# Performance work log

Measured on AMD Instinct MI355X. Metric: run time of the kernel, lower is better.

Reference implementation:

```python
import jax, jax.numpy as jnp
import numpy as np

B, S, D = 1, 2048, 1024
NH, NKV, HD = 16, 4, 64
N_REP = NH // NKV


def _rope_tables(seq_len, half_dim, base=10000.0):
    inv_freq = 1.0 / (base ** (np.arange(0, half_dim, dtype=np.float32) / half_dim))
    t = np.arange(seq_len, dtype=np.float32)
    freqs = np.outer(t, inv_freq)  # (S, HD//2)
    return jnp.asarray(np.cos(freqs)), jnp.asarray(np.sin(freqs))


def setup_inputs() -> dict:
    key = jax.random.key(0)
    ks = jax.random.split(key, 5)
    x = jax.random.normal(ks[0], (B, S, D), dtype=jnp.float32)
    rope_cos, rope_sin = _rope_tables(S, HD // 2)
    sd = 1.0 / np.sqrt(D)
    Wq = jax.random.normal(ks[1], (D, NH * HD), dtype=jnp.float32) * sd
    Wk = jax.random.normal(ks[2], (D, NKV * HD), dtype=jnp.float32) * sd
    Wv = jax.random.normal(ks[3], (D, NKV * HD), dtype=jnp.float32) * sd
    Wo = jax.random.normal(ks[4], (NH * HD, D), dtype=jnp.float32) * sd
    return {"x": x, "rope_cos": rope_cos, "rope_sin": rope_sin,
            "Wq": Wq, "Wk": Wk, "Wv": Wv, "Wo": Wo}


def _apply_rope(t, cos, sin):
    # t: (B, H, S, HD); cos/sin: (S, HD//2). Rotate-half convention.
    t1, t2 = jnp.split(t, 2, axis=-1)
    c = cos[None, None, :, :]
    s = sin[None, None, :, :]
    return jnp.concatenate([t1 * c - t2 * s, t2 * c + t1 * s], axis=-1)


def reference(x, rope_cos, rope_sin, Wq, Wk, Wv, Wo):
    b, s, _ = x.shape
    # projections -> (B, H, S, HD)
    q = (x @ Wq).reshape(b, s, NH, HD).transpose(0, 2, 1, 3)
    k = (x @ Wk).reshape(b, s, NKV, HD).transpose(0, 2, 1, 3)
    v = (x @ Wv).reshape(b, s, NKV, HD).transpose(0, 2, 1, 3)
    q = _apply_rope(q, rope_cos, rope_sin)
    k = _apply_rope(k, rope_cos, rope_sin)
    # GQA expansion (repeat_interleave on head axis)
    k = jnp.repeat(k, N_REP, axis=1)
    v = jnp.repeat(v, N_REP, axis=1)
    scale = HD ** -0.5
    scores = jnp.einsum('bhqd,bhkd->bhqk', q, k) * scale
    causal = jnp.tril(jnp.ones((s, s), dtype=bool))
    scores = jnp.where(causal[None, None], scores, jnp.float32(-jnp.inf))
    attn = jax.nn.softmax(scores, axis=-1)
    out = jnp.einsum('bhqk,bhkd->bhqd', attn, v)  # (B, H, S, HD)
    out = out.transpose(0, 2, 1, 3).reshape(b, s, NH * HD)
    return out @ Wo
```

## Files before the change

### kernel.cpp

```cpp
#include <hip/hip_runtime.h>

typedef unsigned short ushort_t;
typedef __attribute__((ext_vector_type(8))) short short8;
typedef __attribute__((ext_vector_type(4))) float f32x4;
typedef __attribute__((ext_vector_type(4))) unsigned short ushort4v;
typedef __attribute__((ext_vector_type(8))) unsigned short ushort8v;

#define S_LEN 2048
#define D_MODEL 1024
#define NH 16
#define NKV 4
#define HD 64

__device__ __forceinline__ ushort_t f2bf(float f) {
    unsigned u = __float_as_uint(f);
    u += 0x7fffu + ((u >> 16) & 1u);
    return (ushort_t)(u >> 16);
}

__device__ __forceinline__ void cp16(void* lds, const void* g) {
    __builtin_amdgcn_global_load_lds(
        (__attribute__((address_space(1))) void*)g,
        (__attribute__((address_space(3))) void*)lds, 16, 0, 0);
}

__global__ __launch_bounds__(256) void prep_kernel(
    const float* __restrict__ x, ushort_t* __restrict__ xb,
    const float* __restrict__ Wq, const float* __restrict__ Wk,
    const float* __restrict__ Wv, const float* __restrict__ Wo,
    ushort_t* __restrict__ WqT, ushort_t* __restrict__ WkT,
    ushort_t* __restrict__ WvT, ushort_t* __restrict__ WoT)
{
    const int t = threadIdx.x;
    if (blockIdx.z == 4) {
        const int b  = blockIdx.y * 16 + blockIdx.x;
        const int i0 = (b * 256 + t) * 4;
        #pragma unroll
        for (int rep = 0; rep < 8; ++rep) {
            const int i = i0 + rep * 262144;
            float4 v = *(const float4*)(x + i);
            ushort4v o = { f2bf(v.x), f2bf(v.y), f2bf(v.z), f2bf(v.w) };
            *(ushort4v*)(xb + i) = o;
        }
        return;
    }
    __shared__ ushort_t T[64 * 72];
    const float* W; ushort_t* WT; int N;
    switch (blockIdx.z) {
        case 0:  W = Wq; WT = WqT; N = 1024; break;
        case 1:  W = Wk; WT = WkT; N = 256;  break;
        case 2:  W = Wv; WT = WvT; N = 256;  break;
        default: W = Wo; WT = WoT; N = 1024; break;
    }
    const int n0 = blockIdx.y * 64;
    if (n0 >= N) return;
    const int k0 = blockIdx.x * 64;
    const int kr = t >> 4, nc = (t & 15) * 4;
    #pragma unroll
    for (int p = 0; p < 4; ++p) {
        const int k = kr + p * 16;
        float4 v = *(const float4*)(W + (size_t)(k0 + k) * N + n0 + nc);
        T[(nc + 0) * 72 + k] = f2bf(v.x);
        T[(nc + 1) * 72 + k] = f2bf(v.y);
        T[(nc + 2) * 72 + k] = f2bf(v.z);
        T[(nc + 3) * 72 + k] = f2bf(v.w);
    }
    __syncthreads();
    const int n = t >> 2, seg = (t & 3) * 16;
    ushort8v a = *(ushort8v*)&T[n * 72 + seg];
    ushort8v b = *(ushort8v*)&T[n * 72 + seg + 8];
    *(ushort8v*)(WT + (size_t)(n0 + n) * 1024 + k0 + seg)     = a;
    *(ushort8v*)(WT + (size_t)(n0 + n) * 1024 + k0 + seg + 8) = b;
}

__global__ __launch_bounds__(256, 2) void gemm_qkv_mfma(
    const ushort_t* __restrict__ xb, const ushort_t* __restrict__ WqT,
    const ushort_t* __restrict__ WkT, const ushort_t* __restrict__ WvT,
    const float* __restrict__ rc, const float* __restrict__ rs,
    ushort_t* __restrict__ Qb, ushort_t* __restrict__ Kb,
    ushort_t* __restrict__ Vtb)
{
    __shared__ ushort_t As[2][64 * 64];
    __shared__ ushort_t Bs[2][128 * 64];

    const int t = threadIdx.x;
    const int lane = t & 63, wave = t >> 6;
    const int wr = wave >> 1, wc = wave & 1;
    const int quad = lane >> 4, l15 = lane & 15;
    const int lq = lane >> 3, lr = lane & 7;
    const int swz_st = (lr ^ lq) * 8;
    const int l7 = l15 & 7;
    const int fsw0 = (quad ^ l7) * 8;
    const int fsw1 = ((quad + 4) ^ l7) * 8;

    const int m0 = blockIdx.x * 64;
    const int cy = blockIdx.y;

    const ushort_t* WT; int nloc;
    if (cy < 8)       { WT = WqT; nloc = cy * 128; }
    else if (cy < 10) { WT = WkT; nloc = (cy - 8) * 128; }
    else              { WT = WvT; nloc = (cy - 10) * 128; }

    f32x4 acc[2][4];
    #pragma unroll
    for (int i = 0; i < 2; ++i)
        #pragma unroll
        for (int j = 0; j < 4; ++j) acc[i][j] = (f32x4)0.f;

    auto stage = [&](int buf, int k0) {
        #pragma unroll
        for (int i = 0; i < 2; ++i) {
            const int r = wave * 16 + i * 8 + lq;
            cp16(&As[buf][(wave * 16 + i * 8) * 64],
                 xb + (size_t)(m0 + r) * 1024 + k0 + swz_st);
        }
        #pragma unroll
        for (int i = 0; i < 4; ++i) {
            const int r = wave * 32 + i * 8 + lq;
            cp16(&Bs[buf][(wave * 32 + i * 8) * 64],
                 WT + (size_t)(nloc + r) * 1024 + k0 + swz_st);
        }
    };

    stage(0, 0);
    __syncthreads();

    for (int kk = 0; kk < 16; ++kk) {
        const int cur = kk & 1;
        if (kk + 1 < 16) stage(cur ^ 1, (kk + 1) * 64);

        const ushort_t* Ac = &As[cur][0];
        const ushort_t* Bc = &Bs[cur][0];
        #pragma unroll
        for (int h = 0; h < 2; ++h) {
            const int fsw = h ? fsw1 : fsw0;
            short8 av[2], bv[4];
            #pragma unroll
            for (int i = 0; i < 2; ++i)
                av[i] = *(const short8*)&Ac[(wr * 32 + i * 16 + l15) * 64 + fsw];
            #pragma unroll
            for (int j = 0; j < 4; ++j)
                bv[j] = *(const short8*)&Bc[(wc * 64 + j * 16 + l15) * 64 + fsw];
            #pragma unroll
            for (int i = 0; i < 2; ++i)
                #pragma unroll
                for (int j = 0; j < 4; ++j)
                    acc[i][j] = __builtin_amdgcn_mfma_f32_16x16x32_bf16(
                        av[i], bv[j], acc[i][j], 0, 0, 0);
        }
        __syncthreads();
    }

    if (cy < 10) {
        ushort_t* dst = (cy < 8) ? Qb : Kb;
        const int h = ((cy < 8) ? cy : (cy - 8)) * 2 + wc;
        #pragma unroll
        for (int i = 0; i < 2; ++i) {
            #pragma unroll
            for (int j = 0; j < 2; ++j) {
                const int d = j * 16 + l15;
                #pragma unroll
                for (int reg = 0; reg < 4; ++reg) {
                    const int s = m0 + wr * 32 + i * 16 + quad * 4 + reg;
                    const float c  = rc[s * 32 + d];
                    const float sn = rs[s * 32 + d];
                    const float v1 = acc[i][j][reg];
                    const float v2 = acc[i][j + 2][reg];
                    dst[((size_t)h * S_LEN + s) * HD + d]      = f2bf(v1 * c - v2 * sn);
                    dst[((size_t)h * S_LEN + s) * HD + d + 32] = f2bf(v2 * c + v1 * sn);
                }
            }
        }
    } else {
        const int vh = (cy - 10) * 2 + wc;
        #pragma unroll
        for (int i = 0; i < 2; ++i) {
            const int s0 = m0 + wr * 32 + i * 16 + quad * 4;
            #pragma unroll
            for (int j = 0; j < 4; ++j) {
                const int d = j * 16 + l15;
                ushort4v o = { f2bf(acc[i][j][0]), f2bf(acc[i][j][1]),
                               f2bf(acc[i][j][2]), f2bf(acc[i][j][3]) };
                *(ushort4v*)&Vtb[((size_t)vh * HD + d) * S_LEN + s0] = o;
            }
        }
    }
}

__global__ __launch_bounds__(256, 2) void attn_mfma(
    const ushort_t* __restrict__ Qb, const ushort_t* __restrict__ Kb,
    const ushort_t* __restrict__ Vtb, ushort_t* __restrict__ attnb)
{
    __shared__ ushort_t Ks[2][2][64 * 64];
    __shared__ ushort_t Vs[2][2][64 * 64];
    __shared__ ushort_t Ps[4][16 * 72];

    const int t = threadIdx.x;
    const int lane = t & 63, wave = t >> 6;
    const int quad = lane >> 4, l15 = lane & 15;
    const int lq = lane >> 3, lr = lane & 7;
    const int swz_st = (lr ^ lq) * 8;
    const int l7 = l15 & 7;
    const int fsw0 = (quad ^ l7) * 8;
    const int fsw1 = ((quad + 4) ^ l7) * 8;

    const int h  = blockIdx.x;
    const int y  = blockIdx.y;
    const int qt = (y < 16) ? y : 47 - y;
    const int q0 = qt * 64;
    const int kvh = h >> 2;
    const int qrow0 = q0 + wave * 16;

    const ushort_t* Qg = Qb + ((size_t)h * S_LEN + qrow0) * HD;
    const ushort_t* Kg = Kb + (size_t)kvh * S_LEN * HD;
    const ushort_t* Vg = Vtb + (size_t)kvh * HD * S_LEN;

    short8 aq0 = *(const short8*)(Qg + (size_t)l15 * HD + quad * 8);
    short8 aq1 = *(const short8*)(Qg + (size_t)l15 * HD + 32 + quad * 8);

    float ps4[4] = {0.f, 0.f, 0.f, 0.f};
    f32x4 Oacc[4];
    #pragma unroll
    for (int jb = 0; jb < 4; ++jb) Oacc[jb] = (f32x4)0.f;

    const int nround = (qt + 2) >> 1;

    auto stage = [&](int buf, int kvbase) {
        #pragma unroll
        for (int u = 0; u < 2; ++u)
            #pragma unroll
            for (int i = 0; i < 2; ++i) {
                const int r = wave * 16 + i * 8 + lq;
                cp16(&Ks[buf][u][(wave * 16 + i * 8) * 64],
                     Kg + (size_t)(kvbase + u * 64 + r) * 64 + swz_st);
                cp16(&Vs[buf][u][(wave * 16 + i * 8) * 64],
                     Vg + (size_t)r * 2048 + kvbase + u * 64 + swz_st);
            }
    };

    stage(0, 0);
    __syncthreads();

    ushort_t* Pw = &Ps[wave][0];

    for (int round = 0; round < nround; ++round) {
        const int cur = round & 1;
        if (round + 1 < nround) stage(cur ^ 1, (round + 1) * 128);

        #pragma unroll
        for (int u = 0; u < 2; ++u) {
            const int kv0 = round * 128 + u * 64;
            if (kv0 > q0 + 63) break;
            const ushort_t* Kc = &Ks[cur][u][0];
            const ushort_t* Vc = &Vs[cur][u][0];

            f32x4 sv[4];
            #pragma unroll
            for (int jb = 0; jb < 4; ++jb) {
                short8 b0 = *(const short8*)&Kc[(jb * 16 + l15) * 64 + fsw0];
                short8 b1 = *(const short8*)&Kc[(jb * 16 + l15) * 64 + fsw1];
                f32x4 z = (f32x4)0.f;
                z = __builtin_amdgcn_mfma_f32_16x16x32_bf16(aq0, b0, z, 0, 0, 0);
                z = __builtin_amdgcn_mfma_f32_16x16x32_bf16(aq1, b1, z, 0, 0, 0);
                sv[jb] = z;
            }

            const bool diag = (kv0 == q0);
            #pragma unroll
            for (int jb = 0; jb < 4; ++jb) {
                const int col = kv0 + jb * 16 + l15;
                #pragma unroll
                for (int reg = 0; reg < 4; ++reg) {
                    float e = __expf(sv[jb][reg] * 0.125f);
                    if (diag && col > qrow0 + quad * 4 + reg) e = 0.f;
                    sv[jb][reg] = e;
                    ps4[reg] += e;
                }
            }

            #pragma unroll
            for (int jb = 0; jb < 4; ++jb)
                #pragma unroll
                for (int reg = 0; reg < 4; ++reg)
                    Pw[(quad * 4 + reg) * 72 + jb * 16 + l15] = f2bf(sv[jb][reg]);
            short8 p0 = *(const short8*)&Pw[l15 * 72 + quad * 8];
            short8 p1 = *(const short8*)&Pw[l15 * 72 + 32 + quad * 8];

            #pragma unroll
            for (int jb = 0; jb < 4; ++jb) {
                short8 v0 = *(const short8*)&Vc[(jb * 16 + l15) * 64 + fsw0];
                short8 v1 = *(const short8*)&Vc[(jb * 16 + l15) * 64 + fsw1];
                Oacc[jb] = __builtin_amdgcn_mfma_f32_16x16x32_bf16(p0, v0, Oacc[jb], 0, 0, 0);
                Oacc[jb] = __builtin_amdgcn_mfma_f32_16x16x32_bf16(p1, v1, Oacc[jb], 0, 0, 0);
            }
        }

        __syncthreads();
    }

    #pragma unroll
    for (int reg = 0; reg < 4; ++reg) {
        float l = ps4[reg];
        l += __shfl_xor(l, 1);
        l += __shfl_xor(l, 2);
        l += __shfl_xor(l, 4);
        l += __shfl_xor(l, 8);
        const float inv = 1.f / l;
        const int s = qrow0 + quad * 4 + reg;
        #pragma unroll
        for (int jb = 0; jb < 4; ++jb)
            attnb[(size_t)s * D_MODEL + h * HD + jb * 16 + l15] =
                f2bf(Oacc[jb][reg] * inv);
    }
}

__global__ __launch_bounds__(256, 2) void gemm_out_mfma(
    const ushort_t* __restrict__ Ab, const ushort_t* __restrict__ WoT,
    float* __restrict__ out)
{
    __shared__ ushort_t As[2][64 * 64];
    __shared__ ushort_t Bs[2][64 * 64];

    const int t = threadIdx.x;
    const int lane = t & 63, wave = t >> 6;
    const int wr = wave >> 1, wc = wave & 1;
    const int quad = lane >> 4, l15 = lane & 15;
    const int lq = lane >> 3, lr = lane & 7;
    const int swz_st = (lr ^ lq) * 8;
    const int l7 = l15 & 7;
    const int fsw0 = (quad ^ l7) * 8;
    const int fsw1 = ((quad + 4) ^ l7) * 8;

    const int m0 = blockIdx.x * 64;
    const int n0 = blockIdx.y * 64;

    f32x4 acc[2][2];
    #pragma unroll
    for (int i = 0; i < 2; ++i)
        #pragma unroll
        for (int j = 0; j < 2; ++j) acc[i][j] = (f32x4)0.f;

    auto stage = [&](int buf, int k0) {
        #pragma unroll
        for (int i = 0; i < 2; ++i) {
            const int r = wave * 16 + i * 8 + lq;
            cp16(&As[buf][(wave * 16 + i * 8) * 64],
                 Ab + (size_t)(m0 + r) * 1024 + k0 + swz_st);
            cp16(&Bs[buf][(wave * 16 + i * 8) * 64],
                 WoT + (size_t)(n0 + r) * 1024 + k0 + swz_st);
        }
    };

    stage(0, 0);
    __syncthreads();

    for (int kk = 0; kk < 16; ++kk) {
        const int cur = kk & 1;
        if (kk + 1 < 16) stage(cur ^ 1, (kk + 1) * 64);

        const ushort_t* Ac = &As[cur][0];
        const ushort_t* Bc = &Bs[cur][0];
        #pragma unroll
        for (int h = 0; h < 2; ++h) {
            const int fsw = h ? fsw1 : fsw0;
            short8 av[2], bv[2];
            #pragma unroll
            for (int i = 0; i < 2; ++i)
                av[i] = *(const short8*)&Ac[(wr * 32 + i * 16 + l15) * 64 + fsw];
            #pragma unroll
            for (int j = 0; j < 2; ++j)
                bv[j] = *(const short8*)&Bc[(wc * 32 + j * 16 + l15) * 64 + fsw];
            #pragma unroll
            for (int i = 0; i < 2; ++i)
                #pragma unroll
                for (int j = 0; j < 2; ++j)
                    acc[i][j] = __builtin_amdgcn_mfma_f32_16x16x32_bf16(
                        av[i], bv[j], acc[i][j], 0, 0, 0);
        }
        __syncthreads();
    }

    #pragma unroll
    for (int i = 0; i < 2; ++i)
        #pragma unroll
        for (int reg = 0; reg < 4; ++reg) {
            const int s = m0 + wr * 32 + i * 16 + quad * 4 + reg;
            #pragma unroll
            for (int j = 0; j < 2; ++j)
                out[(size_t)s * D_MODEL + n0 + wc * 32 + j * 16 + l15] = acc[i][j][reg];
        }
}

extern "C" void kernel_launch(void* const* d_in, const int* in_sizes, int n_in,
                              void* d_out, int out_size, void* d_ws, size_t ws_size,
                              hipStream_t stream)
{
    const float* x  = (const float*)d_in[0];
    const float* rc = (const float*)d_in[1];
    const float* rs = (const float*)d_in[2];
    const float* Wq = (const float*)d_in[3];
    const float* Wk = (const float*)d_in[4];
    const float* Wv = (const float*)d_in[5];
    const float* Wo = (const float*)d_in[6];
    float* out = (float*)d_out;

    ushort_t* xb   = (ushort_t*)d_ws;
    ushort_t* WqT  = xb   + (size_t)2048 * 1024;
    ushort_t* WkT  = WqT  + (size_t)1024 * 1024;
    ushort_t* WvT  = WkT  + (size_t)256 * 1024;
    ushort_t* WoT  = WvT  + (size_t)256 * 1024;
    ushort_t* Qb   = WoT  + (size_t)1024 * 1024;
    ushort_t* Kb   = Qb   + (size_t)NH * S_LEN * HD;
    ushort_t* Vtb  = Kb   + (size_t)NKV * S_LEN * HD;
    ushort_t* attnb= Vtb  + (size_t)NKV * HD * S_LEN;

    prep_kernel<<<dim3(16, 16, 5), 256, 0, stream>>>(x, xb, Wq, Wk, Wv, Wo,
                                                     WqT, WkT, WvT, WoT);
    gemm_qkv_mfma<<<dim3(32, 12), 256, 0, stream>>>(xb, WqT, WkT, WvT,
                                                    rc, rs, Qb, Kb, Vtb);
    attn_mfma<<<dim3(NH, 32), 256, 0, stream>>>(Qb, Kb, Vtb, attnb);
    gemm_out_mfma<<<dim3(32, 16), 256, 0, stream>>>(attnb, WoT, out);
}
```

Measured before the change: 144.2 us.

## Enlarge GEMM tiles to 128 rows with 8 waves; raise MFMA priority in attention

Both projection GEMMs move from 64-row, 4-wave tiles to 128-row, 8-wave tiles with 512 threads, and the per-wave fragment mapping and RoPE/V epilogues are remapped to match. The larger tiles are meant to improve reuse of the staged weight tile and halve the block count. In the attention kernel, s_setprio brackets the QK and PV MFMA loops so waves in those sections get higher issue priority. The trade-offs are fewer blocks on a large GPU (192 and 256 blocks) and more LDS per block.

```diff
diff --git a/kernel.cpp b/kernel.cpp
--- a/kernel.cpp
+++ b/kernel.cpp
@@ -73,19 +73,19 @@
     *(ushort8v*)(WT + (size_t)(n0 + n) * 1024 + k0 + seg + 8) = b;
 }
 
-__global__ __launch_bounds__(256, 2) void gemm_qkv_mfma(
+__global__ __launch_bounds__(512, 2) void gemm_qkv_mfma(
     const ushort_t* __restrict__ xb, const ushort_t* __restrict__ WqT,
     const ushort_t* __restrict__ WkT, const ushort_t* __restrict__ WvT,
     const float* __restrict__ rc, const float* __restrict__ rs,
     ushort_t* __restrict__ Qb, ushort_t* __restrict__ Kb,
     ushort_t* __restrict__ Vtb)
 {
-    __shared__ ushort_t As[2][64 * 64];
+    __shared__ ushort_t As[2][128 * 64];
     __shared__ ushort_t Bs[2][128 * 64];
 
     const int t = threadIdx.x;
     const int lane = t & 63, wave = t >> 6;
-    const int wr = wave >> 1, wc = wave & 1;
+    const int wr = wave >> 2, wc = wave & 3;
     const int quad = lane >> 4, l15 = lane & 15;
     const int lq = lane >> 3, lr = lane & 7;
     const int swz_st = (lr ^ lq) * 8;
@@ -93,7 +93,7 @@
     const int fsw0 = (quad ^ l7) * 8;
     const int fsw1 = ((quad + 4) ^ l7) * 8;
 
-    const int m0 = blockIdx.x * 64;
+    const int m0 = blockIdx.x * 128;
     const int cy = blockIdx.y;
 
     const ushort_t* WT; int nloc;
@@ -101,24 +101,22 @@
     else if (cy < 10) { WT = WkT; nloc = (cy - 8) * 128; }
     else              { WT = WvT; nloc = (cy - 10) * 128; }
 
-    f32x4 acc[2][4];
-    #pragma unroll
-    for (int i = 0; i < 2; ++i)
-        #pragma unroll
-        for (int j = 0; j < 4; ++j) acc[i][j] = (f32x4)0.f;
+    const int rn0 = (wc >> 1) * 64 + (wc & 1) * 16 + l15;
+    const int rn1 = rn0 + 32;
+    const int ar0 = wr * 64;
+
+    f32x4 acc[4][2];
+    #pragma unroll
+    for (int i = 0; i < 4; ++i)
+        #pragma unroll
+        for (int j = 0; j < 2; ++j) acc[i][j] = (f32x4)0.f;
 
     auto stage = [&](int buf, int k0) {
         #pragma unroll
         for (int i = 0; i < 2; ++i) {
-            const int r = wave * 16 + i * 8 + lq;
-            cp16(&As[buf][(wave * 16 + i * 8) * 64],
-                 xb + (size_t)(m0 + r) * 1024 + k0 + swz_st);
-        }
-        #pragma unroll
-        for (int i = 0; i < 4; ++i) {
-            const int r = wave * 32 + i * 8 + lq;
-            cp16(&Bs[buf][(wave * 32 + i * 8) * 64],
-                 WT + (size_t)(nloc + r) * 1024 + k0 + swz_st);
+            const int r = wave * 16 + i * 8;
+            cp16(&As[buf][r * 64], xb + (size_t)(m0 + r + lq) * 1024 + k0 + swz_st);
+            cp16(&Bs[buf][r * 64], WT + (size_t)(nloc + r + lq) * 1024 + k0 + swz_st);
         }
     };
 
@@ -134,53 +132,50 @@
         #pragma unroll
         for (int h = 0; h < 2; ++h) {
             const int fsw = h ? fsw1 : fsw0;
-            short8 av[2], bv[4];
-            #pragma unroll
-            for (int i = 0; i < 2; ++i)
-                av[i] = *(const short8*)&Ac[(wr * 32 + i * 16 + l15) * 64 + fsw];
-            #pragma unroll
-            for (int j = 0; j < 4; ++j)
-                bv[j] = *(const short8*)&Bc[(wc * 64 + j * 16 + l15) * 64 + fsw];
-            #pragma unroll
-            for (int i = 0; i < 2; ++i)
-                #pragma unroll
-                for (int j = 0; j < 4; ++j)
-                    acc[i][j] = __builtin_amdgcn_mfma_f32_16x16x32_bf16(
-                        av[i], bv[j], acc[i][j], 0, 0, 0);
+            short8 av[4], bv[2];
+            #pragma unroll
+            for (int i = 0; i < 4; ++i)
+                av[i] = *(const short8*)&Ac[(ar0 + i * 16 + l15) * 64 + fsw];
+            bv[0] = *(const short8*)&Bc[rn0 * 64 + fsw];
+            bv[1] = *(const short8*)&Bc[rn1 * 64 + fsw];
+            #pragma unroll
+            for (int i = 0; i < 4; ++i) {
+                acc[i][0] = __builtin_amdgcn_mfma_f32_16x16x32_bf16(
+                    av[i], bv[0], acc[i][0], 0, 0, 0);
+                acc[i][1] = __builtin_amdgcn_mfma_f32_16x16x32_bf16(
+                    av[i], bv[1], acc[i][1], 0, 0, 0);
+            }
         }
         __syncthreads();
     }
 
     if (cy < 10) {
         ushort_t* dst = (cy < 8) ? Qb : Kb;
-        const int h = ((cy < 8) ? cy : (cy - 8)) * 2 + wc;
-        #pragma unroll
-        for (int i = 0; i < 2; ++i) {
-            #pragma unroll
-            for (int j = 0; j < 2; ++j) {
-                const int d = j * 16 + l15;
-                #pragma unroll
-                for (int reg = 0; reg < 4; ++reg) {
-                    const int s = m0 + wr * 32 + i * 16 + quad * 4 + reg;
-                    const float c  = rc[s * 32 + d];
-                    const float sn = rs[s * 32 + d];
-                    const float v1 = acc[i][j][reg];
-                    const float v2 = acc[i][j + 2][reg];
-                    dst[((size_t)h * S_LEN + s) * HD + d]      = f2bf(v1 * c - v2 * sn);
-                    dst[((size_t)h * S_LEN + s) * HD + d + 32] = f2bf(v2 * c + v1 * sn);
-                }
+        const int h = ((cy < 8) ? cy : (cy - 8)) * 2 + (wc >> 1);
+        const int d = (wc & 1) * 16 + l15;
+        #pragma unroll
+        for (int i = 0; i < 4; ++i) {
+            #pragma unroll
+            for (int reg = 0; reg < 4; ++reg) {
+                const int s = m0 + wr * 64 + i * 16 + quad * 4 + reg;
+                const float c  = rc[s * 32 + d];
+                const float sn = rs[s * 32 + d];
+                const float v1 = acc[i][0][reg];
+                const float v2 = acc[i][1][reg];
+                dst[((size_t)h * S_LEN + s) * HD + d]      = f2bf(v1 * c - v2 * sn);
+                dst[((size_t)h * S_LEN + s) * HD + d + 32] = f2bf(v2 * c + v1 * sn);
             }
         }
     } else {
-        const int vh = (cy - 10) * 2 + wc;
-        #pragma unroll
-        for (int i = 0; i < 2; ++i) {
-            const int s0 = m0 + wr * 32 + i * 16 + quad * 4;
-            #pragma unroll
-            for (int j = 0; j < 4; ++j) {
-                const int d = j * 16 + l15;
-                ushort4v o = { f2bf(acc[i][j][0]), f2bf(acc[i][j][1]),
-                               f2bf(acc[i][j][2]), f2bf(acc[i][j][3]) };
+        const int vh = (cy - 10) * 2 + (wc >> 1);
+        #pragma unroll
+        for (int i = 0; i < 4; ++i) {
+            const int s0 = m0 + wr * 64 + i * 16 + quad * 4;
+            #pragma unroll
+            for (int jn = 0; jn < 2; ++jn) {
+                const int d = (wc & 1) * 16 + jn * 32 + l15;
+                ushort4v o = { f2bf(acc[i][jn][0]), f2bf(acc[i][jn][1]),
+                               f2bf(acc[i][jn][2]), f2bf(acc[i][jn][3]) };
                 *(ushort4v*)&Vtb[((size_t)vh * HD + d) * S_LEN + s0] = o;
             }
         }
@@ -255,6 +250,7 @@
             const ushort_t* Vc = &Vs[cur][u][0];
 
             f32x4 sv[4];
+            __builtin_amdgcn_s_setprio(1);
             #pragma unroll
             for (int jb = 0; jb < 4; ++jb) {
                 short8 b0 = *(const short8*)&Kc[(jb * 16 + l15) * 64 + fsw0];
@@ -264,6 +260,7 @@
                 z = __builtin_amdgcn_mfma_f32_16x16x32_bf16(aq1, b1, z, 0, 0, 0);
                 sv[jb] = z;
             }
+            __builtin_amdgcn_s_setprio(0);
 
             const bool diag = (kv0 == q0);
             #pragma unroll
@@ -286,6 +283,7 @@
             short8 p0 = *(const short8*)&Pw[l15 * 72 + quad * 8];
             short8 p1 = *(const short8*)&Pw[l15 * 72 + 32 + quad * 8];
 
+            __builtin_amdgcn_s_setprio(1);
             #pragma unroll
             for (int jb = 0; jb < 4; ++jb) {
                 short8 v0 = *(const short8*)&Vc[(jb * 16 + l15) * 64 + fsw0];
@@ -293,6 +291,7 @@
                 Oacc[jb] = __builtin_amdgcn_mfma_f32_16x16x32_bf16(p0, v0, Oacc[jb], 0, 0, 0);
                 Oacc[jb] = __builtin_amdgcn_mfma_f32_16x16x32_bf16(p1, v1, Oacc[jb], 0, 0, 0);
             }
+            __builtin_amdgcn_s_setprio(0);
         }
 
         __syncthreads();
@@ -314,16 +313,16 @@
     }
 }
 
-__global__ __launch_bounds__(256, 2) void gemm_out_mfma(
+__global__ __launch_bounds__(512, 2) void gemm_out_mfma(
     const ushort_t* __restrict__ Ab, const ushort_t* __restrict__ WoT,
     float* __restrict__ out)
 {
-    __shared__ ushort_t As[2][64 * 64];
+    __shared__ ushort_t As[2][128 * 64];
     __shared__ ushort_t Bs[2][64 * 64];
 
     const int t = threadIdx.x;
     const int lane = t & 63, wave = t >> 6;
-    const int wr = wave >> 1, wc = wave & 1;
+    const int wr = wave >> 2, wc = wave & 3;
     const int quad = lane >> 4, l15 = lane & 15;
     const int lq = lane >> 3, lr = lane & 7;
     const int swz_st = (lr ^ lq) * 8;
@@ -331,24 +330,23 @@
     const int fsw0 = (quad ^ l7) * 8;
     const int fsw1 = ((quad + 4) ^ l7) * 8;
 
-    const int m0 = blockIdx.x * 64;
+    const int m0 = blockIdx.x * 128;
     const int n0 = blockIdx.y * 64;
-
-    f32x4 acc[2][2];
-    #pragma unroll
-    for (int i = 0; i < 2; ++i)
-        #pragma unroll
-        for (int j = 0; j < 2; ++j) acc[i][j] = (f32x4)0.f;
+    const int ar0 = wr * 64;
+    const int brn = wc * 16 + l15;
+
+    f32x4 acc[4];
+    #pragma unroll
+    for (int i = 0; i < 4; ++i) acc[i] = (f32x4)0.f;
 
     auto stage = [&](int buf, int k0) {
         #pragma unroll
         for (int i = 0; i < 2; ++i) {
-            const int r = wave * 16 + i * 8 + lq;
-            cp16(&As[buf][(wave * 16 + i * 8) * 64],
-                 Ab + (size_t)(m0 + r) * 1024 + k0 + swz_st);
-            cp16(&Bs[buf][(wave * 16 + i * 8) * 64],
-                 WoT + (size_t)(n0 + r) * 1024 + k0 + swz_st);
-        }
+            const int r = wave * 16 + i * 8;
+            cp16(&As[buf][r * 64], Ab + (size_t)(m0 + r + lq) * 1024 + k0 + swz_st);
+        }
+        const int rb = wave * 8;
+        cp16(&Bs[buf][rb * 64], WoT + (size_t)(n0 + rb + lq) * 1024 + k0 + swz_st);
     };
 
     stage(0, 0);
@@ -363,31 +361,25 @@
         #pragma unroll
         for (int h = 0; h < 2; ++h) {
             const int fsw = h ? fsw1 : fsw0;
-            short8 av[2], bv[2];
-            #pragma unroll
-            for (int i = 0; i < 2; ++i)
-                av[i] = *(const short8*)&Ac[(wr * 32 + i * 16 + l15) * 64 + fsw];
-            #pragma unroll
-            for (int j = 0; j < 2; ++j)
-                bv[j] = *(const short8*)&Bc[(wc * 32 + j * 16 + l15) * 64 + fsw];
-            #pragma unroll
-            for (int i = 0; i < 2; ++i)
-                #pragma unroll
-                for (int j = 0; j < 2; ++j)
-                    acc[i][j] = __builtin_amdgcn_mfma_f32_16x16x32_bf16(
-                        av[i], bv[j], acc[i][j], 0, 0, 0);
+            short8 av[4], bv;
+            #pragma unroll
+            for (int i = 0; i < 4; ++i)
+                av[i] = *(const short8*)&Ac[(ar0 + i * 16 + l15) * 64 + fsw];
+            bv = *(const short8*)&Bc[brn * 64 + fsw];
+            #pragma unroll
+            for (int i = 0; i < 4; ++i)
+                acc[i] = __builtin_amdgcn_mfma_f32_16x16x32_bf16(
+                    av[i], bv, acc[i], 0, 0, 0);
         }
         __syncthreads();
     }
 
     #pragma unroll
-    for (int i = 0; i < 2; ++i)
+    for (int i = 0; i < 4; ++i)
         #pragma unroll
         for (int reg = 0; reg < 4; ++reg) {
-            const int s = m0 + wr * 32 + i * 16 + quad * 4 + reg;
-            #pragma unroll
-            for (int j = 0; j < 2; ++j)
-                out[(size_t)s * D_MODEL + n0 + wc * 32 + j * 16 + l15] = acc[i][j][reg];
+            const int s = m0 + wr * 64 + i * 16 + quad * 4 + reg;
+            out[(size_t)s * D_MODEL + n0 + wc * 16 + l15] = acc[i][reg];
         }
 }
 
@@ -416,8 +408,8 @@
 
     prep_kernel<<<dim3(16, 16, 5), 256, 0, stream>>>(x, xb, Wq, Wk, Wv, Wo,
                                                      WqT, WkT, WvT, WoT);
-    gemm_qkv_mfma<<<dim3(32, 12), 256, 0, stream>>>(xb, WqT, WkT, WvT,
+    gemm_qkv_mfma<<<dim3(16, 12), 512, 0, stream>>>(xb, WqT, WkT, WvT,
                                                     rc, rs, Qb, Kb, Vtb);
     attn_mfma<<<dim3(NH, 32), 256, 0, stream>>>(Qb, Kb, Vtb, attnb);
-    gemm_out_mfma<<<dim3(32, 16), 256, 0, stream>>>(attnb, WoT, out);
-}
+    gemm_out_mfma<<<dim3(16, 16), 512, 0, stream>>>(attnb, WoT, out);
+}
```

Result: slower. 149.7 us (+3.8%).
